# Kernel tuning notes

Hardware: AMD Instinct MI355X
Metric: run time of the kernel (lower is better)

The kernel has to match this reference:

```python
import jax, jax.numpy as jnp
import numpy as np

N_HEAD = 12

def setup_inputs() -> dict:
    key = jax.random.key(0)
    k1, k2, k3 = jax.random.split(key, 3)
    B, T, C = 8, 1024, 768
    x = jax.random.normal(k1, (B, T, C), dtype=jnp.float32)
    # torch Linear(768, 3*768): store as [in, out] so we can do x @ W
    W_attn = jax.random.normal(k2, (C, 3 * C), dtype=jnp.float32) * 0.02
    b_attn = jax.random.normal(k3, (3 * C,), dtype=jnp.float32) * 0.02
    return {"x": x, "W_attn": W_attn, "b_attn": b_attn}

def reference(x, W_attn, b_attn):
    B, T, C = x.shape
    H = N_HEAD
    hs = C // H
    scale = 1.0 / jnp.sqrt(jnp.asarray(hs, dtype=x.dtype))
    qkv = x @ W_attn + b_attn                      # [B,T,3C]
    q, k, v = jnp.split(qkv, 3, axis=-1)
    q = q.reshape(B, T, H, hs).transpose(0, 2, 1, 3)  # [B,H,T,hs]
    k = k.reshape(B, T, H, hs).transpose(0, 2, 1, 3)
    v = v.reshape(B, T, H, hs).transpose(0, 2, 1, 3)
    scores = jnp.einsum('bhqd,bhkd->bhqk', q, k) * scale
    # causal mask then ReLU (masked -inf entries become 0 after ReLU)
    causal = jnp.tril(jnp.ones((T, T), dtype=bool))
    att = jnp.where(causal[None, None], jax.nn.relu(scores), jnp.zeros((), dtype=scores.dtype))
    out = jnp.einsum('bhqk,bhkd->bhqd', att, v)    # [B,H,T,hs]
    out = out.transpose(0, 2, 1, 3).reshape(B, T, C)
    return out
```

## Files before the change

### kernel.cpp

```cpp
#include <hip/hip_runtime.h>

typedef __attribute__((ext_vector_type(8))) short bf16x8;
typedef __attribute__((ext_vector_type(4))) float f32x4;
typedef __attribute__((ext_vector_type(4))) unsigned short us4;
typedef __attribute__((ext_vector_type(8))) unsigned short us8;

#define MFMA(a, b, c) __builtin_amdgcn_mfma_f32_16x16x32_bf16((a), (b), (c), 0, 0, 0)

__device__ __forceinline__ unsigned short f2bf(float f) {
  unsigned u = __builtin_bit_cast(unsigned, f);
  u = (u + 0x7fffu + ((u >> 16) & 1u)) >> 16;
  return (unsigned short)u;
}

__device__ __forceinline__ void gload16(const void* g, void* l) {
  __builtin_amdgcn_global_load_lds((const __attribute__((address_space(1))) void*)g,
                                   (__attribute__((address_space(3))) void*)l,
                                   16, 0, 0);
}

__device__ __forceinline__ bf16x8 readfrag(const unsigned short* buf, int row, int kbyte) {
  int byte = row * 128 + kbyte;
  byte ^= (row & 7) << 4;
  return *(const bf16x8*)((const char*)buf + byte);
}

__global__ void cast_x_kernel(const float* __restrict__ x,
                              unsigned short* __restrict__ xb, int n4) {
  int id = blockIdx.x * blockDim.x + threadIdx.x;
  if (id >= n4) return;
  float4 v = ((const float4*)x)[id];
  us4 o = { f2bf(v.x), f2bf(v.y), f2bf(v.z), f2bf(v.w) };
  ((us4*)xb)[id] = o;
}

__global__ void castw_kernel(const float* __restrict__ W,
                             unsigned short* __restrict__ Wt) {
  __shared__ unsigned short tile[32][33];
  int bn = blockIdx.x * 32;
  int bk = blockIdx.y * 32;
  int lx = threadIdx.x & 31, ly = threadIdx.x >> 5;
#pragma unroll
  for (int i = 0; i < 32; i += 8)
    tile[ly + i][lx] = f2bf(W[(bk + ly + i) * 2304 + bn + lx]);
  __syncthreads();
#pragma unroll
  for (int i = 0; i < 32; i += 8)
    Wt[(bn + ly + i) * 768 + bk + lx] = tile[lx][ly + i];
}

__global__ __launch_bounds__(512, 2) void qkv_gemm_kernel(
    const unsigned short* __restrict__ xb, const unsigned short* __restrict__ wt,
    const float* __restrict__ bias,
    unsigned short* __restrict__ qb, unsigned short* __restrict__ kb,
    unsigned short* __restrict__ vb) {
  __shared__ unsigned short lds[73728];
  const int tid = threadIdx.x;
  const int lane = tid & 63, wid = tid >> 6;
  const int wm = wid >> 1, wn = wid & 1;
  const int l15 = lane & 15, lg = lane >> 4;

  int bid = blockIdx.x;
  int xcd = bid & 7, c = bid >> 3;
  int mb = (xcd & 3) * 8 + (c & 7);
  int nb = (xcd >> 2) * 9 + (c >> 3);
  const int m0 = mb * 256, n0 = nb * 128;

  const unsigned short* Ab_g = xb + (size_t)m0 * 768;
  const unsigned short* Bb_g = wt + (size_t)n0 * 768;

  int eA[4], sA[4], eB[2], sB[2];
#pragma unroll
  for (int i = 0; i < 4; ++i) {
    int e = (i * 512 + tid) * 8, row = e >> 6;
    eA[i] = e;
    sA[i] = row * 768 + ((e ^ ((row & 7) << 3)) & 63);
  }
#pragma unroll
  for (int i = 0; i < 2; ++i) {
    int e = (i * 512 + tid) * 8, row = e >> 6;
    eB[i] = e;
    sB[i] = row * 768 + ((e ^ ((row & 7) << 3)) & 63);
  }

#define SA(buf, k0, i) gload16(Ab_g + sA[i] + (k0), &lds[(buf) * 16384 + eA[i]])
#define SB(buf, k0, i) gload16(Bb_g + sB[i] + (k0), &lds[49152 + (buf) * 8192 + eB[i]])

  f32x4 acc[4][4] = {};
  bf16x8 bfr[4][2];

  SA(0, 0, 0); SA(0, 0, 1); SA(0, 0, 2); SA(0, 0, 3);
  SB(0, 0, 0); SB(0, 0, 1);
  SA(1, 64, 0); SA(1, 64, 1); SA(1, 64, 2); SA(1, 64, 3);
  SB(1, 64, 0); SB(1, 64, 1);
  asm volatile("s_waitcnt vmcnt(6)" ::: "memory");
  __builtin_amdgcn_s_barrier();

#define GPHASE(cc_, P, STG, EW)                                                   \
  {                                                                               \
    const unsigned short* Abuf = &lds[(cc_) * 16384];                             \
    const unsigned short* Bbuf = &lds[49152 + (cc_) * 8192];                      \
    bf16x8 afr[2][2];                                                             \
    _Pragma("unroll") for (int m2 = 0; m2 < 2; ++m2)                              \
        _Pragma("unroll") for (int kk = 0; kk < 2; ++kk)                          \
            afr[m2][kk] =                                                         \
        readfrag(Abuf, wm * 64 + ((P) * 2 + m2) * 16 + l15, kk * 64 + lg * 16);   \
    if ((P) == 0) {                                                               \
      _Pragma("unroll") for (int nf = 0; nf < 4; ++nf)                            \
          _Pragma("unroll") for (int kk = 0; kk < 2; ++kk)                        \
              bfr[nf][kk] =                                                       \
          readfrag(Bbuf, wn * 64 + nf * 16 + l15, kk * 64 + lg * 16);             \
    }                                                                             \
    STG;                                                                          \
    __builtin_amdgcn_sched_barrier(0);                                            \
    __builtin_amdgcn_s_barrier();                                                 \
    asm volatile("s_waitcnt lgkmcnt(0)" ::: "memory");                            \
    __builtin_amdgcn_sched_barrier(0);                                            \
    __builtin_amdgcn_s_setprio(1);                                                \
    _Pragma("unroll") for (int m2 = 0; m2 < 2; ++m2)                              \
        _Pragma("unroll") for (int nf = 0; nf < 4; ++nf)                          \
            _Pragma("unroll") for (int kk = 0; kk < 2; ++kk)                      \
                acc[(P) * 2 + m2][nf] =                                           \
        MFMA(afr[m2][kk], bfr[nf][kk], acc[(P) * 2 + m2][nf]);                    \
    __builtin_amdgcn_s_setprio(0);                                                \
    EW;                                                                           \
    __builtin_amdgcn_sched_barrier(0);                                            \
    __builtin_amdgcn_s_barrier();                                                 \
  }

  int cc = 0;
  for (int t = 0; t < 10; ++t) {
    int c2 = cc + 2; if (c2 >= 3) c2 -= 3;
    int k2 = (t + 2) * 64;
    GPHASE(cc, 0, { SA(c2, k2, 0); SA(c2, k2, 1); SB(c2, k2, 0); }, );
    GPHASE(cc, 1, { SA(c2, k2, 2); SA(c2, k2, 3); SB(c2, k2, 1); },
           asm volatile("s_waitcnt vmcnt(6)" ::: "memory"));
    cc = (cc == 2) ? 0 : cc + 1;
  }
  GPHASE(cc, 0, , );
  GPHASE(cc, 1, , asm volatile("s_waitcnt vmcnt(0)" ::: "memory"));
  cc = (cc == 2) ? 0 : cc + 1;
  GPHASE(cc, 0, , );
  GPHASE(cc, 1, , );

  __syncthreads();

  const int sec = n0 / 768;
  float bcol[4];
#pragma unroll
  for (int nf = 0; nf < 4; ++nf) bcol[nf] = bias[n0 + wn * 64 + nf * 16 + l15];

  if (sec < 2) {
    unsigned short* ct = lds;
#pragma unroll
    for (int mf = 0; mf < 4; ++mf)
#pragma unroll
      for (int nf = 0; nf < 4; ++nf)
#pragma unroll
        for (int r = 0; r < 4; ++r)
          ct[(wm * 64 + mf * 16 + lg * 4 + r) * 128 + wn * 64 + nf * 16 + l15] =
              f2bf(acc[mf][nf][r] + bcol[nf]);
    __syncthreads();
    unsigned short* dstbase = (sec == 0) ? qb : kb;
    const int hbase = (n0 - sec * 768) >> 6;
    const int g8 = tid >> 3, l8 = tid & 7;
#pragma unroll
    for (int j = 0; j < 8; ++j) {
      int chunk = j * 64 + g8;
      int row = chunk >> 1, hh = chunk & 1;
      us8 v = *(const us8*)&ct[row * 128 + hh * 64 + l8 * 8];
      int t = m0 + row, bb = t >> 10, tt = t & 1023;
      *(us8*)(dstbase + ((size_t)((bb * 12 + hbase + hh) * 1024 + tt)) * 64 + l8 * 8) = v;
    }
  } else {
#pragma unroll
    for (int nf = 0; nf < 4; ++nf) {
      int cc2 = (n0 - 1536) + wn * 64 + nf * 16 + l15;
      int h = cc2 >> 6, d = cc2 & 63;
#pragma unroll
      for (int mf = 0; mf < 4; ++mf) {
        int row0 = m0 + wm * 64 + mf * 16 + lg * 4;
        int bb = row0 >> 10, t0 = row0 & 1023;
        us4 o;
#pragma unroll
        for (int r = 0; r < 4; ++r) o[r] = f2bf(acc[mf][nf][r] + bcol[nf]);
        *(us4*)(vb + ((size_t)((bb * 12 + h) * 64 + d)) * 1024 + t0) = o;
      }
    }
  }
#undef SA
#undef SB
#undef GPHASE
}

__global__ __launch_bounds__(512, 2) void attn_kernel(
    const unsigned short* __restrict__ qb, const unsigned short* __restrict__ kb,
    const unsigned short* __restrict__ vb, float* __restrict__ out) {
  __shared__ unsigned short lds[65536];
  const int tid = threadIdx.x;
  const int lane = tid & 63, wid = tid >> 6;
  const int qs = wid >> 1, ks = wid & 1;
  const int l15 = lane & 15, lg = lane >> 4;

  int bid = blockIdx.x;
  int xcd = bid & 7, c = bid >> 3;
  int bh = xcd * 12 + (c % 12);
  int byq = 3 - (c / 12);
  const int b = bh / 12, h = bh % 12;
  const size_t base = (size_t)bh * 65536;
  const int Q = byq * 4 + qs;
  const int qr0 = byq * 256 + qs * 64;

  bf16x8 aq[4][2];
#pragma unroll
  for (int mf = 0; mf < 4; ++mf)
#pragma unroll
    for (int kk = 0; kk < 2; ++kk)
      aq[mf][kk] = *(const bf16x8*)(qb + base + (size_t)(qr0 + mf * 16 + l15) * 64 +
                                    kk * 32 + lg * 8);

  const int e = tid * 8;
  const int row = e >> 6;
  const int esw = e ^ ((row & 7) << 3);

#define ASTAGE(buf, i_)                                                            \
  {                                                                                \
    int kt0 = 2 * (i_);                                                            \
    gload16(kb + base + (size_t)kt0 * 4096 + esw, &lds[(buf) * 8192 + e]);         \
    gload16(kb + base + (size_t)(kt0 + 1) * 4096 + esw,                            \
            &lds[(buf) * 8192 + 4096 + e]);                                        \
    gload16(vb + base + (size_t)row * 1024 + kt0 * 64 + (esw & 63),                \
            &lds[16384 + (buf) * 8192 + e]);                                       \
    gload16(vb + base + (size_t)row * 1024 + (kt0 + 1) * 64 + (esw & 63),          \
            &lds[16384 + (buf) * 8192 + 4096 + e]);                                \
  }

  f32x4 o[4][4] = {};
  unsigned short* Sb = &lds[32768 + wid * 4096];

  const int niter = 2 * byq + 2;
  ASTAGE(0, 0);
  asm volatile("s_waitcnt vmcnt(0)" ::: "memory");
  __builtin_amdgcn_s_barrier();

  for (int i = 0; i < niter; ++i) {
    const int cur = i & 1;
    if (i + 1 < niter) ASTAGE(cur ^ 1, i + 1);
    const int kt = 2 * i + ks;
    if (kt <= Q) {
      const unsigned short* Kb = &lds[cur * 8192 + ks * 4096];
      const unsigned short* Vb = &lds[16384 + cur * 8192 + ks * 4096];
      bf16x8 bk[4][2];
#pragma unroll
      for (int nf = 0; nf < 4; ++nf)
#pragma unroll
        for (int kk = 0; kk < 2; ++kk)
          bk[nf][kk] = readfrag(Kb, nf * 16 + l15, kk * 64 + lg * 16);
      const bool diag = (kt == Q);
      __builtin_amdgcn_s_setprio(1);
#pragma unroll
      for (int mf = 0; mf < 4; ++mf)
#pragma unroll
        for (int nf = 0; nf < 4; ++nf) {
          f32x4 s = {};
          s = MFMA(aq[mf][0], bk[nf][0], s);
          s = MFMA(aq[mf][1], bk[nf][1], s);
          int colk = nf * 16 + l15;
#pragma unroll
          for (int r = 0; r < 4; ++r) {
            int rowq = mf * 16 + lg * 4 + r;
            float v = fmaxf(s[r] * 0.125f, 0.0f);
            if (diag && colk > rowq) v = 0.0f;
            int byte = (rowq * 128 + colk * 2) ^ ((rowq & 7) << 4);
            *(unsigned short*)((char*)Sb + byte) = f2bf(v);
          }
        }
      __builtin_amdgcn_s_setprio(0);
      bf16x8 pa[4][2];
#pragma unroll
      for (int mf = 0; mf < 4; ++mf)
#pragma unroll
        for (int kk = 0; kk < 2; ++kk)
          pa[mf][kk] = readfrag(Sb, mf * 16 + l15, kk * 64 + lg * 16);
      __builtin_amdgcn_s_setprio(1);
#pragma unroll
      for (int mf = 0; mf < 4; ++mf)
#pragma unroll
        for (int df = 0; df < 4; ++df)
#pragma unroll
          for (int kk = 0; kk < 2; ++kk)
            o[mf][df] = MFMA(pa[mf][kk], readfrag(Vb, df * 16 + l15, kk * 64 + lg * 16),
                             o[mf][df]);
      __builtin_amdgcn_s_setprio(0);
    }
    asm volatile("s_waitcnt vmcnt(0)" ::: "memory");
    __builtin_amdgcn_sched_barrier(0);
    __builtin_amdgcn_s_barrier();
  }
#undef ASTAGE

  float* fr = (float*)lds;
  if (ks == 1) {
#pragma unroll
    for (int mf = 0; mf < 4; ++mf)
#pragma unroll
      for (int df = 0; df < 4; ++df)
#pragma unroll
        for (int r = 0; r < 4; ++r) {
          int rowq = mf * 16 + lg * 4 + r, col = df * 16 + l15;
          int idx = (qs * 4096 + rowq * 64 + col) ^ ((rowq & 4) << 2);
          fr[idx] = o[mf][df][r];
        }
  }
  __syncthreads();
  if (ks == 0) {
#pragma unroll
    for (int mf = 0; mf < 4; ++mf)
#pragma unroll
      for (int df = 0; df < 4; ++df)
#pragma unroll
        for (int r = 0; r < 4; ++r) {
          int rowq = mf * 16 + lg * 4 + r, col = df * 16 + l15;
          int idx = (qs * 4096 + rowq * 64 + col) ^ ((rowq & 4) << 2);
          float v = o[mf][df][r] + fr[idx];
          out[(size_t)(b * 1024 + qr0 + rowq) * 768 + h * 64 + col] = v;
        }
  }
}

extern "C" void kernel_launch(void* const* d_in, const int* in_sizes, int n_in,
                              void* d_out, int out_size, void* d_ws, size_t ws_size,
                              hipStream_t stream) {
  const float* x = (const float*)d_in[0];
  const float* W = (const float*)d_in[1];
  const float* bias = (const float*)d_in[2];
  float* out = (float*)d_out;

  unsigned short* xb = (unsigned short*)d_ws;
  unsigned short* wt = xb + 6291456;
  unsigned short* qb = wt + 1769472;
  unsigned short* kb = qb + 6291456;
  unsigned short* vb = kb + 6291456;

  cast_x_kernel<<<6144, 256, 0, stream>>>(x, xb, 1572864);
  castw_kernel<<<dim3(72, 24), 256, 0, stream>>>(W, wt);
  qkv_gemm_kernel<<<576, 512, 0, stream>>>(xb, wt, bias, qb, kb, vb);
  attn_kernel<<<384, 512, 0, stream>>>(qb, kb, vb, out);
}
```

Baseline: 98.92 us.

## Shrink QKV GEMM tile to 128x128 with 256 threads and decoupled A/B buffering

Changes the QKV projection GEMM from 256x128 tiles with 512 threads to 128x128 tiles with 256 threads, doubling the grid to 1152 blocks. The pipeline is restructured so A keeps triple buffering while B uses double buffering with its own stage schedule, and LDS use drops to 40960 shorts. The aim is better occupancy and load balance across CUs. The cost is less data reuse per block and more global traffic for the weight tiles.

```diff
diff --git a/kernel.cpp b/kernel.cpp
--- a/kernel.cpp
+++ b/kernel.cpp
@@ -49,12 +49,12 @@
     Wt[(bn + ly + i) * 768 + bk + lx] = tile[lx][ly + i];
 }
 
-__global__ __launch_bounds__(512, 2) void qkv_gemm_kernel(
+__global__ __launch_bounds__(256, 2) void qkv_gemm_kernel(
     const unsigned short* __restrict__ xb, const unsigned short* __restrict__ wt,
     const float* __restrict__ bias,
     unsigned short* __restrict__ qb, unsigned short* __restrict__ kb,
     unsigned short* __restrict__ vb) {
-  __shared__ unsigned short lds[73728];
+  __shared__ unsigned short lds[40960];
   const int tid = threadIdx.x;
   const int lane = tid & 63, wid = tid >> 6;
   const int wm = wid >> 1, wn = wid & 1;
@@ -62,44 +62,37 @@
 
   int bid = blockIdx.x;
   int xcd = bid & 7, c = bid >> 3;
-  int mb = (xcd & 3) * 8 + (c & 7);
-  int nb = (xcd >> 2) * 9 + (c >> 3);
-  const int m0 = mb * 256, n0 = nb * 128;
+  int mb = xcd * 8 + (c & 7);
+  int nb = c >> 3;
+  const int m0 = mb * 128, n0 = nb * 128;
 
   const unsigned short* Ab_g = xb + (size_t)m0 * 768;
   const unsigned short* Bb_g = wt + (size_t)n0 * 768;
 
-  int eA[4], sA[4], eB[2], sB[2];
+  int eA[4], sA[4];
 #pragma unroll
   for (int i = 0; i < 4; ++i) {
-    int e = (i * 512 + tid) * 8, row = e >> 6;
+    int e = (i * 256 + tid) * 8, row = e >> 6;
     eA[i] = e;
     sA[i] = row * 768 + ((e ^ ((row & 7) << 3)) & 63);
   }
-#pragma unroll
-  for (int i = 0; i < 2; ++i) {
-    int e = (i * 512 + tid) * 8, row = e >> 6;
-    eB[i] = e;
-    sB[i] = row * 768 + ((e ^ ((row & 7) << 3)) & 63);
-  }
-
-#define SA(buf, k0, i) gload16(Ab_g + sA[i] + (k0), &lds[(buf) * 16384 + eA[i]])
-#define SB(buf, k0, i) gload16(Bb_g + sB[i] + (k0), &lds[49152 + (buf) * 8192 + eB[i]])
+
+#define SA(buf, k0, i) gload16(Ab_g + sA[i] + (k0), &lds[(buf) * 8192 + eA[i]])
+#define SB(buf, k0, i) gload16(Bb_g + sA[i] + (k0), &lds[24576 + (buf) * 8192 + eA[i]])
 
   f32x4 acc[4][4] = {};
   bf16x8 bfr[4][2];
 
   SA(0, 0, 0); SA(0, 0, 1); SA(0, 0, 2); SA(0, 0, 3);
-  SB(0, 0, 0); SB(0, 0, 1);
+  SB(0, 0, 0); SB(0, 0, 1); SB(0, 0, 2); SB(0, 0, 3);
   SA(1, 64, 0); SA(1, 64, 1); SA(1, 64, 2); SA(1, 64, 3);
-  SB(1, 64, 0); SB(1, 64, 1);
-  asm volatile("s_waitcnt vmcnt(6)" ::: "memory");
+  asm volatile("s_waitcnt vmcnt(4)" ::: "memory");
   __builtin_amdgcn_s_barrier();
 
-#define GPHASE(cc_, P, STG, EW)                                                   \
+#define GPHASE(cA_, cB_, P, STG, EW)                                              \
   {                                                                               \
-    const unsigned short* Abuf = &lds[(cc_) * 16384];                             \
-    const unsigned short* Bbuf = &lds[49152 + (cc_) * 8192];                      \
+    const unsigned short* Abuf = &lds[(cA_) * 8192];                              \
+    const unsigned short* Bbuf = &lds[24576 + (cB_) * 8192];                      \
     bf16x8 afr[2][2];                                                             \
     _Pragma("unroll") for (int m2 = 0; m2 < 2; ++m2)                              \
         _Pragma("unroll") for (int kk = 0; kk < 2; ++kk)                          \
@@ -128,20 +121,21 @@
     __builtin_amdgcn_s_barrier();                                                 \
   }
 
-  int cc = 0;
+  int cA = 0;
   for (int t = 0; t < 10; ++t) {
-    int c2 = cc + 2; if (c2 >= 3) c2 -= 3;
-    int k2 = (t + 2) * 64;
-    GPHASE(cc, 0, { SA(c2, k2, 0); SA(c2, k2, 1); SB(c2, k2, 0); }, );
-    GPHASE(cc, 1, { SA(c2, k2, 2); SA(c2, k2, 3); SB(c2, k2, 1); },
-           asm volatile("s_waitcnt vmcnt(6)" ::: "memory"));
-    cc = (cc == 2) ? 0 : cc + 1;
-  }
-  GPHASE(cc, 0, , );
-  GPHASE(cc, 1, , asm volatile("s_waitcnt vmcnt(0)" ::: "memory"));
-  cc = (cc == 2) ? 0 : cc + 1;
-  GPHASE(cc, 0, , );
-  GPHASE(cc, 1, , );
+    int cB = t & 1, cBn = cB ^ 1;
+    int cA2 = cA + 2; if (cA2 >= 3) cA2 -= 3;
+    int k1 = (t + 1) * 64, k2 = (t + 2) * 64;
+    GPHASE(cA, cB, 0, { SB(cBn, k1, 0); SB(cBn, k1, 1); SB(cBn, k1, 2); SB(cBn, k1, 3); }, );
+    GPHASE(cA, cB, 1, { SA(cA2, k2, 0); SA(cA2, k2, 1); SA(cA2, k2, 2); SA(cA2, k2, 3); },
+           asm volatile("s_waitcnt vmcnt(4)" ::: "memory"));
+    cA = (cA == 2) ? 0 : cA + 1;
+  }
+  GPHASE(cA, 0, 0, { SB(1, 704, 0); SB(1, 704, 1); SB(1, 704, 2); SB(1, 704, 3); }, );
+  GPHASE(cA, 0, 1, , asm volatile("s_waitcnt vmcnt(0)" ::: "memory"));
+  cA = (cA == 2) ? 0 : cA + 1;
+  GPHASE(cA, 1, 0, , );
+  GPHASE(cA, 1, 1, , );
 
   __syncthreads();
 
@@ -166,7 +160,7 @@
     const int g8 = tid >> 3, l8 = tid & 7;
 #pragma unroll
     for (int j = 0; j < 8; ++j) {
-      int chunk = j * 64 + g8;
+      int chunk = j * 32 + g8;
       int row = chunk >> 1, hh = chunk & 1;
       us8 v = *(const us8*)&ct[row * 128 + hh * 64 + l8 * 8];
       int t = m0 + row, bb = t >> 10, tt = t & 1023;
@@ -344,6 +338,6 @@
 
   cast_x_kernel<<<6144, 256, 0, stream>>>(x, xb, 1572864);
   castw_kernel<<<dim3(72, 24), 256, 0, stream>>>(W, wt);
-  qkv_gemm_kernel<<<576, 512, 0, stream>>>(xb, wt, bias, qb, kb, vb);
+  qkv_gemm_kernel<<<1152, 256, 0, stream>>>(xb, wt, bias, qb, kb, vb);
   attn_kernel<<<384, 512, 0, stream>>>(qb, kb, vb, out);
 }
```

Result: faster. 87.00 us (-12.1%).
